# Performance work log

Measured on AMD Instinct MI355X. Metric: run time of the kernel, lower is better.

Reference implementation:

```python
import jax, jax.numpy as jnp
import numpy as np

CTX = 2048
D_IN = 2048
D_OUT = 2048
N_HEADS = 16
HEAD_DIM = D_OUT // N_HEADS
ROPE_BASE = 10000.0


def rope_tables(head_dim, ctx):
    inv_freq = 1.0 / (ROPE_BASE ** (jnp.arange(0, head_dim, 2, dtype=jnp.float32) / head_dim))
    angles = jnp.arange(ctx, dtype=jnp.float32)[:, None] * inv_freq[None, :]  # [ctx, hd/2]
    angles = jnp.concatenate([angles, angles], axis=1)  # [ctx, hd]
    return jnp.sin(angles), jnp.cos(angles)


def apply_rope(x, sin, cos):
    # x: [b, h, s, d]; rotate-by-half (Raschka / Llama style)
    s = x.shape[2]
    d = x.shape[3]
    x1, x2 = x[..., : d // 2], x[..., d // 2 :]
    rotated = jnp.concatenate([-x2, x1], axis=-1)
    return x * cos[:s][None, None] + rotated * sin[:s][None, None]


def setup_inputs() -> dict:
    key = jax.random.key(0)
    kx, kq, kk, kv, ko = jax.random.split(key, 5)
    scale = 0.02
    return {
        "x": jax.random.normal(kx, (2, CTX, D_IN), dtype=jnp.float32),
        "W_query": jax.random.normal(kq, (D_IN, D_OUT), dtype=jnp.float32) * scale,
        "W_key": jax.random.normal(kk, (D_IN, D_OUT), dtype=jnp.float32) * scale,
        "W_value": jax.random.normal(kv, (D_IN, D_OUT), dtype=jnp.float32) * scale,
        "W_out": jax.random.normal(ko, (D_OUT, D_OUT), dtype=jnp.float32) * scale,
    }


def reference(x, W_query, W_key, W_value, W_out):
    bs, cl, _ = x.shape
    sin, cos = rope_tables(HEAD_DIM, CTX)

    def split_heads(t):  # [b, s, d_out] -> [b, h, s, hd]
        return t.reshape(bs, cl, N_HEADS, HEAD_DIM).transpose(0, 2, 1, 3)

    q = split_heads(x @ W_query)
    k = split_heads(x @ W_key)
    v = split_heads(x @ W_value)

    q = apply_rope(q, sin, cos)
    k = apply_rope(k, sin, cos)

    # NOTE: original module does NOT scale by 1/sqrt(head_dim)
    scores = jnp.einsum("bhqd,bhkd->bhqk", q, k)
    causal = jnp.triu(jnp.ones((cl, cl), dtype=bool), k=1)
    scores = jnp.where(causal[None, None], -jnp.inf, scores)
    weights = jax.nn.softmax(scores, axis=-1)
    ctx = jnp.einsum("bhqk,bhkd->bhqd", weights, v)
    ctx = ctx.transpose(0, 2, 1, 3).reshape(bs, cl, N_HEADS * HEAD_DIM)
    return ctx @ W_out
```

## Files before the change

### kernel.cpp

```cpp
#include <hip/hip_runtime.h>
#include <cstdint>
#include <cstddef>

typedef _Float16 f16;
typedef _Float16 f16x8 __attribute__((ext_vector_type(8)));
typedef _Float16 f16x4 __attribute__((ext_vector_type(4)));
typedef float    f32x4 __attribute__((ext_vector_type(4)));

#define S_CTX 2048
#define NH 16
#define DH 128

#define BAR() asm volatile("s_barrier" ::: "memory")
#define VMW(n) asm volatile("s_waitcnt vmcnt(" #n ")" ::: "memory")
#define MF(a, b, c) __builtin_amdgcn_mfma_f32_16x16x32_f16((a), (b), (c), 0, 0, 0)

__device__ __forceinline__ void gload16(const void* g, void* l) {
  __builtin_amdgcn_global_load_lds(
      (const __attribute__((address_space(1))) void*)g,
      (__attribute__((address_space(3))) void*)l, 16, 0, 0);
}

__global__ void prep(const float* __restrict__ x,
                     const float* __restrict__ w0, const float* __restrict__ w1,
                     const float* __restrict__ w2, const float* __restrict__ w3,
                     f16* __restrict__ xb,
                     f16* __restrict__ o0, f16* __restrict__ o1,
                     f16* __restrict__ o2, f16* __restrict__ o3,
                     float* __restrict__ sint, float* __restrict__ cost) {
  const int bid = blockIdx.x, tid = threadIdx.x;
  if (bid < 512) {
    int idx = bid * 256 + tid;
    int j = idx & 63, s = idx >> 6;
    float invf = __expf(-(float)(2 * j) * (1.0f / 128.0f) * 9.210340371976184f);
    float a = (float)s * invf;
    sint[idx] = sinf(a);
    cost[idx] = cosf(a);
  } else if (bid < 8704) {
    int i = ((bid - 512) * 256 + tid) * 4;
    float4 v = *(const float4*)(x + i);
    f16x4 o; o[0] = (f16)v.x; o[1] = (f16)v.y; o[2] = (f16)v.z; o[3] = (f16)v.w;
    *(f16x4*)(xb + i) = o;
  } else {
    int b2 = bid - 8704;
    int z = b2 >> 12, rem = b2 & 4095;
    int by = rem >> 6, bx = rem & 63;
    int tx = tid & 31, ty = tid >> 5;
    const float* in; f16* out;
    switch (z) {
      case 0: in = w0; out = o0; break;
      case 1: in = w1; out = o1; break;
      case 2: in = w2; out = o2; break;
      default: in = w3; out = o3; break;
    }
    __shared__ float tl[32][33];
    int xc = bx * 32 + tx, yc = by * 32 + ty;
#pragma unroll
    for (int r = 0; r < 32; r += 8)
      tl[ty + r][tx] = in[(size_t)(yc + r) * 2048 + xc];
    __syncthreads();
    int xo = by * 32 + tx, yo = bx * 32 + ty;
#pragma unroll
    for (int r = 0; r < 32; r += 8)
      out[(size_t)(yo + r) * 2048 + xo] = (f16)tl[tx][ty + r];
  }
}

__global__ __launch_bounds__(512, 1)
void gemm_qk(const f16* __restrict__ A, const f16* __restrict__ wqT,
             const f16* __restrict__ wkT,
             f16* __restrict__ qb, f16* __restrict__ kb,
             const float* __restrict__ sint, const float* __restrict__ cost) {
  extern __shared__ __align__(16) char lds[];
  const int tid = threadIdx.x, lane = tid & 63;
  const int wvi = tid >> 6, wm = wvi >> 2, wn = wvi & 3;
  const int gcol = blockIdx.x * 256;
  const int proj = gcol >> 11;
  const int col0 = gcol & 2047;
  const int row0 = blockIdx.y * 256;
  const f16* Bt = proj ? wkT : wqT;

  const int ca0 = tid, ca1 = tid + 512;
  const int ra0 = ca0 >> 2, ra1 = ca1 >> 2;
  const int sa0 = (ca0 & 3) ^ ((ra0 >> 1) & 3);
  const int sa1 = (ca1 & 3) ^ ((ra1 >> 1) & 3);
  const f16* gA0 = A + (size_t)(row0 + ra0) * 2048 + sa0 * 8;
  const f16* gA1 = A + (size_t)(row0 + ra1) * 2048 + sa1 * 8;
  const f16* gB0 = Bt + (size_t)(col0 + ra0) * 2048 + sa0 * 8;
  const f16* gB1 = Bt + (size_t)(col0 + ra1) * 2048 + sa1 * 8;

  const int kslot = lane >> 4;
  int aoff[8], boff[4];
#pragma unroll
  for (int i = 0; i < 8; i++) {
    int row = wm * 128 + i * 16 + (lane & 15);
    aoff[i] = row * 64 + ((kslot ^ ((row >> 1) & 3)) << 4);
  }
#pragma unroll
  for (int j = 0; j < 4; j++) {
    int rb = (wn >> 1) * 128 + (wn & 1) * 32 + (j & 1) * 16 + (j >> 1) * 64 + (lane & 15);
    boff[j] = rb * 64 + ((kslot ^ ((rb >> 1) & 3)) << 4);
  }

  f32x4 acc[8][4] = {};

#define QKPH(SLOT, HS, SSLOT, DOSTAGE, WN) do {                                \
    const char* As_ = lds + (SLOT) * 32768;                                    \
    const char* Bs_ = As_ + 16384;                                             \
    f16x8 af[8], bf[4];                                                        \
    _Pragma("unroll") for (int i_ = 0; i_ < 8; i_++)                           \
      af[i_] = *(const f16x8*)(As_ + aoff[i_]);                                \
    _Pragma("unroll") for (int j_ = 0; j_ < 4; j_++)                           \
      bf[j_] = *(const f16x8*)(Bs_ + boff[j_]);                                \
    if (DOSTAGE) {                                                             \
      char* dA = lds + (SSLOT) * 32768;                                        \
      gload16(gA0 + (HS) * 32, dA + ca0 * 16);                                 \
      gload16(gA1 + (HS) * 32, dA + ca1 * 16);                                 \
      gload16(gB0 + (HS) * 32, dA + 16384 + ca0 * 16);                         \
      gload16(gB1 + (HS) * 32, dA + 16384 + ca1 * 16);                         \
    }                                                                          \
    asm volatile("s_waitcnt vmcnt(" #WN ")" ::: "memory");                     \
    BAR();                                                                     \
    __builtin_amdgcn_s_setprio(1);                                             \
    _Pragma("unroll") for (int i_ = 0; i_ < 8; i_++)                           \
      _Pragma("unroll") for (int j_ = 0; j_ < 4; j_++)                         \
        acc[i_][j_] = MF(af[i_], bf[j_], acc[i_][j_]);                         \
    __builtin_amdgcn_s_setprio(0);                                             \
    BAR();                                                                     \
  } while (0)

#pragma unroll
  for (int h = 0; h < 2; h++) {
    char* dA = lds + h * 32768;
    gload16(gA0 + h * 32, dA + ca0 * 16);
    gload16(gA1 + h * 32, dA + ca1 * 16);
    gload16(gB0 + h * 32, dA + 16384 + ca0 * 16);
    gload16(gB1 + h * 32, dA + 16384 + ca1 * 16);
  }
  VMW(4); BAR();

  for (int t = 0; t < 20; ++t) {
    const int hb = 3 * t;
    QKPH(0, hb + 2, 2, 1, 4);
    QKPH(1, hb + 3, 0, 1, 4);
    QKPH(2, hb + 4, 1, 1, 4);
  }
  QKPH(0, 62, 2, 1, 4);
  QKPH(1, 63, 0, 1, 4);
  QKPH(2, 0, 0, 0, 0);
  QKPH(0, 0, 0, 0, 63);
#undef QKPH

  const int b = row0 >> 11, sb = row0 & 2047;
  f16* dst = proj ? kb : qb;
  const int h = (col0 >> 7) + (wn >> 1);
#pragma unroll
  for (int i = 0; i < 8; i++)
#pragma unroll
    for (int jj = 0; jj < 2; jj++)
#pragma unroll
      for (int r = 0; r < 4; r++) {
        int s = sb + wm * 128 + i * 16 + (lane >> 4) * 4 + r;
        int d = (wn & 1) * 32 + jj * 16 + (lane & 15);
        float cv = cost[s * 64 + d], sv = sint[s * 64 + d];
        float x1 = acc[i][jj][r], x2 = acc[i][jj + 2][r];
        size_t base = ((size_t)(b * NH + h) * S_CTX + s) << 7;
        dst[base + d]      = (f16)(x1 * cv - x2 * sv);
        dst[base + d + 64] = (f16)(x2 * cv + x1 * sv);
      }
}

template<int MODE>
__global__ __launch_bounds__(512, 1)
void gemm8(const f16* __restrict__ A, const f16* __restrict__ Bt,
           f16* __restrict__ vtb, float* __restrict__ of) {
  extern __shared__ __align__(16) char lds[];
#define RING_A(e) (lds + (e) * 16384)
#define RING_B(e) (lds + 65536 + (e) * 8192)
  const int tid = threadIdx.x, lane = tid & 63;
  const int wvi = tid >> 6, wm = wvi >> 1, wn = wvi & 1;
  const int col0 = blockIdx.x * 128;
  const int row0 = blockIdx.y * 256;

  const int ca0 = tid, ca1 = tid + 512, cb0 = tid;
  const int rAs0 = ca0 >> 2, rAs1 = ca1 >> 2, rBs0 = cb0 >> 2;
  const int sA0 = (ca0 & 3) ^ ((rAs0 >> 1) & 3);
  const int sA1 = (ca1 & 3) ^ ((rAs1 >> 1) & 3);
  const int sB0 = (cb0 & 3) ^ ((rBs0 >> 1) & 3);
  const f16* gA0 = A + (size_t)(row0 + rAs0) * 2048 + sA0 * 8;
  const f16* gA1 = A + (size_t)(row0 + rAs1) * 2048 + sA1 * 8;
  const f16* gB0 = Bt + (size_t)(col0 + rBs0) * 2048 + sB0 * 8;

  const int kslot = lane >> 4;
  int aoff[4], boff[4];
#pragma unroll
  for (int i = 0; i < 4; i++) {
    int row = wm * 64 + i * 16 + (lane & 15);
    aoff[i] = row * 64 + ((kslot ^ ((row >> 1) & 3)) << 4);
  }
#pragma unroll
  for (int j = 0; j < 4; j++) {
    int rb = wn * 32 + (j & 1) * 16 + (j >> 1) * 64 + (lane & 15);
    boff[j] = rb * 64 + ((kslot ^ ((rb >> 1) & 3)) << 4);
  }

  f32x4 acc[4][4] = {};

#define PH8(SLOT, HS, DOSTAGE, WN) do {                                        \
    const char* As_ = RING_A(SLOT);                                            \
    const char* Bs_ = RING_B(SLOT);                                            \
    f16x8 af[4], bf[4];                                                        \
    _Pragma("unroll") for (int i_ = 0; i_ < 4; i_++)                           \
      af[i_] = *(const f16x8*)(As_ + aoff[i_]);                                \
    _Pragma("unroll") for (int j_ = 0; j_ < 4; j_++)                           \
      bf[j_] = *(const f16x8*)(Bs_ + boff[j_]);                                \
    if (DOSTAGE) {                                                             \
      gload16(gA0 + (HS) * 32, RING_A((HS) & 3) + ca0 * 16);                   \
      gload16(gA1 + (HS) * 32, RING_A((HS) & 3) + ca1 * 16);                   \
      gload16(gB0 + (HS) * 32, RING_B((HS) & 3) + cb0 * 16);                   \
    }                                                                          \
    asm volatile("s_waitcnt vmcnt(" #WN ")" ::: "memory");                     \
    BAR();                                                                     \
    __builtin_amdgcn_s_setprio(1);                                             \
    _Pragma("unroll") for (int i_ = 0; i_ < 4; i_++)                           \
      _Pragma("unroll") for (int j_ = 0; j_ < 4; j_++)                         \
        acc[i_][j_] = MF(af[i_], bf[j_], acc[i_][j_]);                         \
    __builtin_amdgcn_s_setprio(0);                                             \
    BAR();                                                                     \
  } while (0)

#pragma unroll
  for (int h = 0; h < 3; h++) {
    gload16(gA0 + h * 32, RING_A(h) + ca0 * 16);
    gload16(gA1 + h * 32, RING_A(h) + ca1 * 16);
    gload16(gB0 + h * 32, RING_B(h) + cb0 * 16);
  }
  VMW(6); BAR();

  for (int t = 0; t < 15; ++t) {
    const int p = t * 4;
    PH8(0, p + 3, 1, 6);
    PH8(1, p + 4, 1, 6);
    PH8(2, p + 5, 1, 6);
    PH8(3, p + 6, 1, 6);
  }
  PH8(0, 63, 1, 6);
  PH8(1, 0, 0, 3);
  PH8(2, 0, 0, 0);
  PH8(3, 0, 0, 63);
#undef PH8

  const int b = row0 >> 11, sbase = row0 & 2047;

  if (MODE == 2) {
#pragma unroll
    for (int i = 0; i < 4; i++)
#pragma unroll
      for (int j = 0; j < 4; j++)
#pragma unroll
        for (int r = 0; r < 4; r++) {
          int row = row0 + wm * 64 + i * 16 + (lane >> 4) * 4 + r;
          int col = col0 + wn * 32 + (j & 1) * 16 + (j >> 1) * 64 + (lane & 15);
          of[(size_t)row * 2048 + col] = acc[i][j][r];
        }
  } else {
    const int h = col0 >> 7;
    f16x4* ldsv = (f16x4*)lds;
#pragma unroll
    for (int i = 0; i < 4; i++)
#pragma unroll
      for (int j = 0; j < 4; j++) {
        f16x4 v;
#pragma unroll
        for (int r = 0; r < 4; r++) v[r] = (f16)acc[i][j][r];
        int su = wm * 16 + i * 4 + (lane >> 4);
        int d  = wn * 32 + (j & 1) * 16 + (j >> 1) * 64 + (lane & 15);
        ldsv[d * 64 + (su ^ ((d << 1) & 63))] = v;
      }
    __syncthreads();
#pragma unroll
    for (int it = 0; it < 8; ++it) {
      int o = it * 512 + tid;
      int d = o >> 5, c = o & 31;
      int xc = (d << 1) & 63;
      f16x4 lo = ldsv[d * 64 + ((2 * c) ^ xc)];
      f16x4 hi = ldsv[d * 64 + ((2 * c + 1) ^ xc)];
      f16x8 vv;
      vv[0] = lo[0]; vv[1] = lo[1]; vv[2] = lo[2]; vv[3] = lo[3];
      vv[4] = hi[0]; vv[5] = hi[1]; vv[6] = hi[2]; vv[7] = hi[3];
      *(f16x8*)&vtb[((size_t)(b * NH + h) * DH + d) * S_CTX + sbase + c * 8] = vv;
    }
  }
#undef RING_A
#undef RING_B
}

__global__ __launch_bounds__(512)
void attn_k(const f16* __restrict__ q, const f16* __restrict__ kk,
            const f16* __restrict__ vt, f16* __restrict__ ctx) {
  __shared__ __align__(16) f16 Ks[2][64 * 128];
  __shared__ __align__(16) f16 Vs[2][128 * 64];
  __shared__ __align__(16) f16 Pl[8][16 * 64];
  const int tid = threadIdx.x, lane = tid & 63, wv = tid >> 6;
  const int bid = blockIdx.x;
  const int xcd = bid & 7, rr = bid >> 3;
  const int bh = xcd + 8 * (rr & 3);
  const int qp = rr >> 2;
  const int b = bh >> 4, h = bh & 15;
  const size_t plane = (size_t)bh * (S_CTX * DH);
  const f16* Qp = q + plane;
  const f16* Kp = kk + plane;
  const f16* Vp = vt + plane;
  const float LOG2E = 1.4426950408889634f;

  const int ck0 = tid, ck1 = tid + 512;
  const int cv0 = tid, cv1 = tid + 512;

  for (int half = 0; half < 2; half++) {
    const int Q = half ? (15 - qp) : qp;
    const int q0 = Q * 128;
    const int NT = 2 * Q + 2;

    f16x8 qf[4];
    {
      const f16* qq = Qp + (size_t)(q0 + wv * 16 + (lane & 15)) * DH + ((lane >> 4) * 8);
#pragma unroll
      for (int ks = 0; ks < 4; ks++) {
        qf[ks] = *(const f16x8*)(qq + ks * 32);
#pragma unroll
        for (int e = 0; e < 8; e++) qf[ks][e] = (f16)((float)qf[ks][e] * LOG2E);
      }
    }
    float m_[4], l_[4];
    f32x4 o[8] = {};
#pragma unroll
    for (int r = 0; r < 4; r++) { m_[r] = -3e38f; l_[r] = 0.f; }

    {
      int rk0 = ck0 >> 4, rk1 = ck1 >> 4;
      gload16(Kp + (size_t)rk0 * DH + (((ck0 & 15) ^ (rk0 & 7)) * 8), &Ks[0][ck0 * 8]);
      gload16(Kp + (size_t)rk1 * DH + (((ck1 & 15) ^ (rk1 & 7)) * 8), &Ks[0][ck1 * 8]);
      int rv0 = cv0 >> 3, rv1 = cv1 >> 3;
      gload16(Vp + (size_t)rv0 * S_CTX + (((cv0 & 7) ^ (rv0 & 7)) * 8), &Vs[0][cv0 * 8]);
      gload16(Vp + (size_t)rv1 * S_CTX + (((cv1 & 7) ^ (rv1 & 7)) * 8), &Vs[0][cv1 * 8]);
    }
    VMW(0); BAR();

    int cur = 0;
    for (int t = 0; t < NT; t++) {
      if (t + 1 < NT) {
        const f16* Kt = Kp + (size_t)(t + 1) * 64 * DH;
        const f16* Vt = Vp + (size_t)(t + 1) * 64;
        int nb = cur ^ 1;
        int rk0 = ck0 >> 4, rk1 = ck1 >> 4;
        gload16(Kt + (size_t)rk0 * DH + (((ck0 & 15) ^ (rk0 & 7)) * 8), &Ks[nb][ck0 * 8]);
        gload16(Kt + (size_t)rk1 * DH + (((ck1 & 15) ^ (rk1 & 7)) * 8), &Ks[nb][ck1 * 8]);
        int rv0 = cv0 >> 3, rv1 = cv1 >> 3;
        gload16(Vt + (size_t)rv0 * S_CTX + (((cv0 & 7) ^ (rv0 & 7)) * 8), &Vs[nb][cv0 * 8]);
        gload16(Vt + (size_t)rv1 * S_CTX + (((cv1 & 7) ^ (rv1 & 7)) * 8), &Vs[nb][cv1 * 8]);
      }

      const f16* Ksc = Ks[cur];
      const f16* Vsc = Vs[cur];

      f32x4 st[4] = {};
      __builtin_amdgcn_s_setprio(1);
#pragma unroll
      for (int n = 0; n < 4; n++) {
        int rK = n * 16 + (lane & 15);
#pragma unroll
        for (int ks = 0; ks < 4; ks++) {
          int slot = ks * 4 + (lane >> 4);
          f16x8 kf = *(const f16x8*)&Ksc[rK * 128 + ((slot ^ (rK & 7)) << 3)];
          st[n] = MF(qf[ks], kf, st[n]);
        }
      }
      __builtin_amdgcn_s_setprio(0);
      if (t >= 2 * Q) {
#pragma unroll
        for (int n = 0; n < 4; n++)
#pragma unroll
          for (int r = 0; r < 4; r++) {
            int kvc = t * 64 + n * 16 + (lane & 15);
            int qr = q0 + wv * 16 + (lane >> 4) * 4 + r;
            if (kvc > qr) st[n][r] = -3e38f;
          }
      }
      float mx[4];
#pragma unroll
      for (int r = 0; r < 4; r++)
        mx[r] = fmaxf(fmaxf(st[0][r], st[1][r]), fmaxf(st[2][r], st[3][r]));
#pragma unroll
      for (int msk = 1; msk < 16; msk <<= 1)
#pragma unroll
        for (int r = 0; r < 4; r++) mx[r] = fmaxf(mx[r], __shfl_xor(mx[r], msk));
      bool need = false;
#pragma unroll
      for (int r = 0; r < 4; r++) need = need || (mx[r] > m_[r] + 8.0f);
      if (__any(need)) {
#pragma unroll
        for (int r = 0; r < 4; r++) {
          float nm = fmaxf(m_[r], mx[r]);
          float al = __builtin_amdgcn_exp2f(m_[r] - nm);
          m_[r] = nm;
          l_[r] *= al;
#pragma unroll
          for (int j = 0; j < 8; j++) o[j][r] *= al;
        }
      }
      float ps[4] = {0.f, 0.f, 0.f, 0.f};
      float pvv[4][4];
#pragma unroll
      for (int n = 0; n < 4; n++)
#pragma unroll
        for (int r = 0; r < 4; r++) {
          float p = __builtin_amdgcn_exp2f(st[n][r] - m_[r]);
          pvv[n][r] = p; ps[r] += p;
        }
#pragma unroll
      for (int msk = 1; msk < 16; msk <<= 1)
#pragma unroll
        for (int r = 0; r < 4; r++) ps[r] += __shfl_xor(ps[r], msk);
#pragma unroll
      for (int r = 0; r < 4; r++) l_[r] += ps[r];

      f16* Pw = Pl[wv];
#pragma unroll
      for (int n = 0; n < 4; n++)
#pragma unroll
        for (int r = 0; r < 4; r++) {
          int rowp = (lane >> 4) * 4 + r;
          int colp = n * 16 + (lane & 15);
          Pw[rowp * 64 + (((colp >> 3) ^ (rowp & 7)) << 3) + (colp & 7)] = (f16)pvv[n][r];
        }
      __builtin_amdgcn_s_setprio(1);
#pragma unroll
      for (int ks = 0; ks < 2; ks++) {
        int rowp = lane & 15;
        int slotp = ks * 4 + (lane >> 4);
        f16x8 pa = *(const f16x8*)&Pw[rowp * 64 + ((slotp ^ (rowp & 7)) << 3)];
#pragma unroll
        for (int j = 0; j < 8; j++) {
          int rv = j * 16 + (lane & 15);
          int slotv = ks * 4 + (lane >> 4);
          f16x8 vf = *(const f16x8*)&Vsc[rv * 64 + ((slotv ^ (rv & 7)) << 3)];
          o[j] = MF(pa, vf, o[j]);
        }
      }
      __builtin_amdgcn_s_setprio(0);

      VMW(0); BAR();
      cur ^= 1;
    }

#pragma unroll
    for (int j = 0; j < 8; j++)
#pragma unroll
      for (int r = 0; r < 4; r++) {
        int qr = q0 + wv * 16 + (lane >> 4) * 4 + r;
        int dd = h * 128 + j * 16 + (lane & 15);
        ctx[((size_t)(b * S_CTX + qr) * 2048) + dd] = (f16)(o[j][r] / l_[r]);
      }
  }
}

extern "C" void kernel_launch(void* const* d_in, const int* in_sizes, int n_in,
                              void* d_out, int out_size, void* d_ws, size_t ws_size,
                              hipStream_t stream) {
  (void)in_sizes; (void)n_in; (void)out_size; (void)ws_size;
  const float* x  = (const float*)d_in[0];
  const float* Wq = (const float*)d_in[1];
  const float* Wk = (const float*)d_in[2];
  const float* Wv = (const float*)d_in[3];
  const float* Wo = (const float*)d_in[4];
  float* out = (float*)d_out;
  char* ws = (char*)d_ws;

  f16*   xb   = (f16*)(ws);
  f16*   ctxb = (f16*)(ws);
  f16*   wqT  = (f16*)(ws + 16777216);
  f16*   wkT  = (f16*)(ws + 25165824);
  f16*   wvT  = (f16*)(ws + 33554432);
  f16*   woT  = (f16*)(ws + 41943040);
  f16*   qb   = (f16*)(ws + 50331648);
  f16*   kb   = (f16*)(ws + 67108864);
  f16*   vtb  = (f16*)(ws + 83886080);
  float* sint = (float*)(ws + 100663296);
  float* cost = (float*)(ws + 101187584);

  prep<<<dim3(25088), dim3(256), 0, stream>>>(x, Wq, Wk, Wv, Wo, xb,
                                              wqT, wkT, wvT, woT, sint, cost);
  gemm_qk<<<dim3(16, 16), dim3(512), 98304, stream>>>(xb, wqT, wkT, qb, kb, sint, cost);
  gemm8<1><<<dim3(16, 16), dim3(512), 98304, stream>>>(xb, wvT, vtb, nullptr);
  attn_k<<<dim3(256), dim3(512), 0, stream>>>(qb, kb, vtb, ctxb);
  gemm8<2><<<dim3(16, 16), dim3(512), 98304, stream>>>(ctxb, woT, nullptr, out);
}
```

Before: 273.4 us.

## Rewrite attention with 32x32 MFMA, register-resident P, and per-block q-tile grid

The attention kernel moves from 16x16x32 to 32x32x16 MFMA and computes S transposed (K times Q), so the P fragments can be packed to f16 and rearranged with v_permlane32_swap in registers instead of going through a per-wave LDS scratch buffer. Blocks shrink to 4 waves of 32 query rows each, and the grid doubles to 512 blocks with one q-tile per block, replacing the paired causal-balancing loop, with launch bounds asking for 2 blocks per CU. This cuts LDS traffic and shuffle reductions, but drops the explicit load balancing of causal tiles and relies on the hardware scheduler and occupancy instead.

```diff
diff --git a/kernel.cpp b/kernel.cpp
--- a/kernel.cpp
+++ b/kernel.cpp
@@ -6,6 +6,8 @@
 typedef _Float16 f16x8 __attribute__((ext_vector_type(8)));
 typedef _Float16 f16x4 __attribute__((ext_vector_type(4)));
 typedef float    f32x4 __attribute__((ext_vector_type(4)));
+typedef float    f32x16 __attribute__((ext_vector_type(16)));
+typedef int      i32x4 __attribute__((ext_vector_type(4)));
 
 #define S_CTX 2048
 #define NH 16
@@ -14,11 +16,20 @@
 #define BAR() asm volatile("s_barrier" ::: "memory")
 #define VMW(n) asm volatile("s_waitcnt vmcnt(" #n ")" ::: "memory")
 #define MF(a, b, c) __builtin_amdgcn_mfma_f32_16x16x32_f16((a), (b), (c), 0, 0, 0)
+#define MF32(a, b, c) __builtin_amdgcn_mfma_f32_32x32x16_f16((a), (b), (c), 0, 0, 0)
 
 __device__ __forceinline__ void gload16(const void* g, void* l) {
   __builtin_amdgcn_global_load_lds(
       (const __attribute__((address_space(1))) void*)g,
       (__attribute__((address_space(3))) void*)l, 16, 0, 0);
+}
+
+__device__ __forceinline__ int pk2(float a, float b) {
+  auto hv = __builtin_amdgcn_cvt_pkrtz(a, b);
+  return __builtin_bit_cast(int, hv);
+}
+__device__ __forceinline__ void pl_swap(int& a, int& b) {
+  asm volatile("v_permlane32_swap_b32 %0, %1" : "+v"(a), "+v"(b));
 }
 
 __global__ void prep(const float* __restrict__ x,
@@ -295,172 +306,157 @@
 #undef RING_B
 }
 
-__global__ __launch_bounds__(512)
+__global__ __launch_bounds__(256, 2)
 void attn_k(const f16* __restrict__ q, const f16* __restrict__ kk,
             const f16* __restrict__ vt, f16* __restrict__ ctx) {
   __shared__ __align__(16) f16 Ks[2][64 * 128];
   __shared__ __align__(16) f16 Vs[2][128 * 64];
-  __shared__ __align__(16) f16 Pl[8][16 * 64];
   const int tid = threadIdx.x, lane = tid & 63, wv = tid >> 6;
+  const int lh = lane >> 5, q31 = lane & 31;
   const int bid = blockIdx.x;
   const int xcd = bid & 7, rr = bid >> 3;
   const int bh = xcd + 8 * (rr & 3);
-  const int qp = rr >> 2;
+  const int Q = 15 - (rr >> 2);
   const int b = bh >> 4, h = bh & 15;
   const size_t plane = (size_t)bh * (S_CTX * DH);
   const f16* Qp = q + plane;
   const f16* Kp = kk + plane;
   const f16* Vp = vt + plane;
   const float LOG2E = 1.4426950408889634f;
-
-  const int ck0 = tid, ck1 = tid + 512;
-  const int cv0 = tid, cv1 = tid + 512;
-
-  for (int half = 0; half < 2; half++) {
-    const int Q = half ? (15 - qp) : qp;
-    const int q0 = Q * 128;
-    const int NT = 2 * Q + 2;
-
-    f16x8 qf[4];
+  const int q0 = Q * 128;
+  const int NT = 2 * Q + 2;
+
+#define STAGE(T, BUF) do {                                                      \
+    const f16* Kt = Kp + (size_t)(T) * 64 * DH;                                 \
+    const f16* Vt = Vp + (size_t)(T) * 64;                                      \
+    _Pragma("unroll") for (int j_ = 0; j_ < 4; j_++) {                          \
+      int c = tid + j_ * 256; int rk = c >> 4;                                  \
+      gload16(Kt + (size_t)rk * DH + (((c & 15) ^ (rk & 7)) * 8), &Ks[BUF][c * 8]); \
+    }                                                                           \
+    _Pragma("unroll") for (int j_ = 0; j_ < 4; j_++) {                          \
+      int c = tid + j_ * 256; int rv = c >> 3;                                  \
+      gload16(Vt + (size_t)rv * S_CTX + (((c & 7) ^ (rv & 7)) * 8), &Vs[BUF][c * 8]); \
+    }                                                                           \
+  } while (0)
+
+  f16x8 qf[8];
+  {
+    const f16* qq = Qp + (size_t)(q0 + wv * 32 + q31) * DH + lh * 8;
+#pragma unroll
+    for (int s = 0; s < 8; s++) {
+      qf[s] = *(const f16x8*)(qq + s * 16);
+#pragma unroll
+      for (int e = 0; e < 8; e++) qf[s][e] = (f16)((float)qf[s][e] * LOG2E);
+    }
+  }
+  float m_ = -3e38f, l_ = 0.f;
+  f32x16 o[4] = {};
+
+  STAGE(0, 0);
+  VMW(0); BAR();
+
+  int cur = 0;
+  for (int t = 0; t < NT; t++) {
+    if (t + 1 < NT) {
+      if (cur) STAGE(t + 1, 0); else STAGE(t + 1, 1);
+    }
+    const f16* Ksc = Ks[cur];
+    const f16* Vsc = Vs[cur];
+
+    f32x16 st0 = {}, st1 = {};
+    __builtin_amdgcn_s_setprio(1);
+#pragma unroll
+    for (int s = 0; s < 8; s++) {
+      const int r0 = q31, r1 = 32 + q31;
+      f16x8 kf0 = *(const f16x8*)&Ksc[r0 * 128 + (((2 * s + lh) ^ (r0 & 7)) << 3)];
+      f16x8 kf1 = *(const f16x8*)&Ksc[r1 * 128 + (((2 * s + lh) ^ (r1 & 7)) << 3)];
+      st0 = MF32(kf0, qf[s], st0);
+      st1 = MF32(kf1, qf[s], st1);
+    }
+    __builtin_amdgcn_s_setprio(0);
+
+    if (t >= 2 * Q) {
+      const int qg = q0 + wv * 32 + q31;
+#pragma unroll
+      for (int r = 0; r < 16; r++) {
+        int kvb = t * 64 + (r & 3) + 8 * (r >> 2) + 4 * lh;
+        if (kvb > qg) st0[r] = -3e38f;
+        if (kvb + 32 > qg) st1[r] = -3e38f;
+      }
+    }
+    float mx = st0[0];
+#pragma unroll
+    for (int r = 1; r < 16; r++) mx = fmaxf(mx, st0[r]);
+#pragma unroll
+    for (int r = 0; r < 16; r++) mx = fmaxf(mx, st1[r]);
+    mx = fmaxf(mx, __shfl_xor(mx, 32));
+    if (__any(mx > m_ + 8.0f)) {
+      float nm = fmaxf(m_, mx);
+      float al = __builtin_amdgcn_exp2f(m_ - nm);
+      m_ = nm; l_ *= al;
+#pragma unroll
+      for (int r = 0; r < 16; r++) {
+        float alr = __shfl(al, (r & 3) + 8 * (r >> 2) + 4 * lh);
+#pragma unroll
+        for (int j = 0; j < 4; j++) o[j][r] *= alr;
+      }
+    }
+    float s_ = 0.f;
+#pragma unroll
+    for (int r = 0; r < 16; r++) { st0[r] = __builtin_amdgcn_exp2f(st0[r] - m_); s_ += st0[r]; }
+#pragma unroll
+    for (int r = 0; r < 16; r++) { st1[r] = __builtin_amdgcn_exp2f(st1[r] - m_); s_ += st1[r]; }
+    s_ += __shfl_xor(s_, 32);
+    l_ += s_;
+
+    f16x8 pa[4];
     {
-      const f16* qq = Qp + (size_t)(q0 + wv * 16 + (lane & 15)) * DH + ((lane >> 4) * 8);
-#pragma unroll
-      for (int ks = 0; ks < 4; ks++) {
-        qf[ks] = *(const f16x8*)(qq + ks * 32);
-#pragma unroll
-        for (int e = 0; e < 8; e++) qf[ks][e] = (f16)((float)qf[ks][e] * LOG2E);
+      int w0 = pk2(st0[0], st0[1]),   w1 = pk2(st0[2], st0[3]);
+      int w2 = pk2(st0[4], st0[5]),   w3 = pk2(st0[6], st0[7]);
+      int w4 = pk2(st0[8], st0[9]),   w5 = pk2(st0[10], st0[11]);
+      int w6 = pk2(st0[12], st0[13]), w7 = pk2(st0[14], st0[15]);
+      pl_swap(w0, w2); pl_swap(w1, w3); pl_swap(w4, w6); pl_swap(w5, w7);
+      i32x4 a = {w0, w1, w2, w3}; pa[0] = __builtin_bit_cast(f16x8, a);
+      i32x4 bb = {w4, w5, w6, w7}; pa[1] = __builtin_bit_cast(f16x8, bb);
+    }
+    {
+      int w0 = pk2(st1[0], st1[1]),   w1 = pk2(st1[2], st1[3]);
+      int w2 = pk2(st1[4], st1[5]),   w3 = pk2(st1[6], st1[7]);
+      int w4 = pk2(st1[8], st1[9]),   w5 = pk2(st1[10], st1[11]);
+      int w6 = pk2(st1[12], st1[13]), w7 = pk2(st1[14], st1[15]);
+      pl_swap(w0, w2); pl_swap(w1, w3); pl_swap(w4, w6); pl_swap(w5, w7);
+      i32x4 a = {w0, w1, w2, w3}; pa[2] = __builtin_bit_cast(f16x8, a);
+      i32x4 bb = {w4, w5, w6, w7}; pa[3] = __builtin_bit_cast(f16x8, bb);
+    }
+
+    __builtin_amdgcn_s_setprio(1);
+#pragma unroll
+    for (int j = 0; j < 4; j++) {
+      const int rv = 32 * j + q31;
+#pragma unroll
+      for (int s2 = 0; s2 < 4; s2++) {
+        f16x8 vf = *(const f16x8*)&Vsc[rv * 64 + (((2 * s2 + lh) ^ (rv & 7)) << 3)];
+        o[j] = MF32(pa[s2], vf, o[j]);
       }
     }
-    float m_[4], l_[4];
-    f32x4 o[8] = {};
-#pragma unroll
-    for (int r = 0; r < 4; r++) { m_[r] = -3e38f; l_[r] = 0.f; }
-
-    {
-      int rk0 = ck0 >> 4, rk1 = ck1 >> 4;
-      gload16(Kp + (size_t)rk0 * DH + (((ck0 & 15) ^ (rk0 & 7)) * 8), &Ks[0][ck0 * 8]);
-      gload16(Kp + (size_t)rk1 * DH + (((ck1 & 15) ^ (rk1 & 7)) * 8), &Ks[0][ck1 * 8]);
-      int rv0 = cv0 >> 3, rv1 = cv1 >> 3;
-      gload16(Vp + (size_t)rv0 * S_CTX + (((cv0 & 7) ^ (rv0 & 7)) * 8), &Vs[0][cv0 * 8]);
-      gload16(Vp + (size_t)rv1 * S_CTX + (((cv1 & 7) ^ (rv1 & 7)) * 8), &Vs[0][cv1 * 8]);
-    }
+    __builtin_amdgcn_s_setprio(0);
+
     VMW(0); BAR();
-
-    int cur = 0;
-    for (int t = 0; t < NT; t++) {
-      if (t + 1 < NT) {
-        const f16* Kt = Kp + (size_t)(t + 1) * 64 * DH;
-        const f16* Vt = Vp + (size_t)(t + 1) * 64;
-        int nb = cur ^ 1;
-        int rk0 = ck0 >> 4, rk1 = ck1 >> 4;
-        gload16(Kt + (size_t)rk0 * DH + (((ck0 & 15) ^ (rk0 & 7)) * 8), &Ks[nb][ck0 * 8]);
-        gload16(Kt + (size_t)rk1 * DH + (((ck1 & 15) ^ (rk1 & 7)) * 8), &Ks[nb][ck1 * 8]);
-        int rv0 = cv0 >> 3, rv1 = cv1 >> 3;
-        gload16(Vt + (size_t)rv0 * S_CTX + (((cv0 & 7) ^ (rv0 & 7)) * 8), &Vs[nb][cv0 * 8]);
-        gload16(Vt + (size_t)rv1 * S_CTX + (((cv1 & 7) ^ (rv1 & 7)) * 8), &Vs[nb][cv1 * 8]);
-      }
-
-      const f16* Ksc = Ks[cur];
-      const f16* Vsc = Vs[cur];
-
-      f32x4 st[4] = {};
-      __builtin_amdgcn_s_setprio(1);
-#pragma unroll
-      for (int n = 0; n < 4; n++) {
-        int rK = n * 16 + (lane & 15);
-#pragma unroll
-        for (int ks = 0; ks < 4; ks++) {
-          int slot = ks * 4 + (lane >> 4);
-          f16x8 kf = *(const f16x8*)&Ksc[rK * 128 + ((slot ^ (rK & 7)) << 3)];
-          st[n] = MF(qf[ks], kf, st[n]);
-        }
-      }
-      __builtin_amdgcn_s_setprio(0);
-      if (t >= 2 * Q) {
-#pragma unroll
-        for (int n = 0; n < 4; n++)
-#pragma unroll
-          for (int r = 0; r < 4; r++) {
-            int kvc = t * 64 + n * 16 + (lane & 15);
-            int qr = q0 + wv * 16 + (lane >> 4) * 4 + r;
-            if (kvc > qr) st[n][r] = -3e38f;
-          }
-      }
-      float mx[4];
-#pragma unroll
-      for (int r = 0; r < 4; r++)
-        mx[r] = fmaxf(fmaxf(st[0][r], st[1][r]), fmaxf(st[2][r], st[3][r]));
-#pragma unroll
-      for (int msk = 1; msk < 16; msk <<= 1)
-#pragma unroll
-        for (int r = 0; r < 4; r++) mx[r] = fmaxf(mx[r], __shfl_xor(mx[r], msk));
-      bool need = false;
-#pragma unroll
-      for (int r = 0; r < 4; r++) need = need || (mx[r] > m_[r] + 8.0f);
-      if (__any(need)) {
-#pragma unroll
-        for (int r = 0; r < 4; r++) {
-          float nm = fmaxf(m_[r], mx[r]);
-          float al = __builtin_amdgcn_exp2f(m_[r] - nm);
-          m_[r] = nm;
-          l_[r] *= al;
-#pragma unroll
-          for (int j = 0; j < 8; j++) o[j][r] *= al;
-        }
-      }
-      float ps[4] = {0.f, 0.f, 0.f, 0.f};
-      float pvv[4][4];
-#pragma unroll
-      for (int n = 0; n < 4; n++)
-#pragma unroll
-        for (int r = 0; r < 4; r++) {
-          float p = __builtin_amdgcn_exp2f(st[n][r] - m_[r]);
-          pvv[n][r] = p; ps[r] += p;
-        }
-#pragma unroll
-      for (int msk = 1; msk < 16; msk <<= 1)
-#pragma unroll
-        for (int r = 0; r < 4; r++) ps[r] += __shfl_xor(ps[r], msk);
-#pragma unroll
-      for (int r = 0; r < 4; r++) l_[r] += ps[r];
-
-      f16* Pw = Pl[wv];
-#pragma unroll
-      for (int n = 0; n < 4; n++)
-#pragma unroll
-        for (int r = 0; r < 4; r++) {
-          int rowp = (lane >> 4) * 4 + r;
-          int colp = n * 16 + (lane & 15);
-          Pw[rowp * 64 + (((colp >> 3) ^ (rowp & 7)) << 3) + (colp & 7)] = (f16)pvv[n][r];
-        }
-      __builtin_amdgcn_s_setprio(1);
-#pragma unroll
-      for (int ks = 0; ks < 2; ks++) {
-        int rowp = lane & 15;
-        int slotp = ks * 4 + (lane >> 4);
-        f16x8 pa = *(const f16x8*)&Pw[rowp * 64 + ((slotp ^ (rowp & 7)) << 3)];
-#pragma unroll
-        for (int j = 0; j < 8; j++) {
-          int rv = j * 16 + (lane & 15);
-          int slotv = ks * 4 + (lane >> 4);
-          f16x8 vf = *(const f16x8*)&Vsc[rv * 64 + ((slotv ^ (rv & 7)) << 3)];
-          o[j] = MF(pa, vf, o[j]);
-        }
-      }
-      __builtin_amdgcn_s_setprio(0);
-
-      VMW(0); BAR();
-      cur ^= 1;
-    }
-
-#pragma unroll
-    for (int j = 0; j < 8; j++)
-#pragma unroll
-      for (int r = 0; r < 4; r++) {
-        int qr = q0 + wv * 16 + (lane >> 4) * 4 + r;
-        int dd = h * 128 + j * 16 + (lane & 15);
-        ctx[((size_t)(b * S_CTX + qr) * 2048) + dd] = (f16)(o[j][r] / l_[r]);
-      }
+    cur ^= 1;
+  }
+#undef STAGE
+
+  float inv = 1.0f / l_;
+#pragma unroll
+  for (int r = 0; r < 16; r++) {
+    int crow = (r & 3) + 8 * (r >> 2) + 4 * lh;
+    float invr = __shfl(inv, crow);
+    int qg = q0 + wv * 32 + crow;
+#pragma unroll
+    for (int j = 0; j < 4; j++) {
+      int dd = h * 128 + 32 * j + q31;
+      ctx[((size_t)(b * S_CTX + qg) * 2048) + dd] = (f16)(o[j][r] * invr);
+    }
   }
 }
 
@@ -492,6 +488,6 @@
                                               wqT, wkT, wvT, woT, sint, cost);
   gemm_qk<<<dim3(16, 16), dim3(512), 98304, stream>>>(xb, wqT, wkT, qb, kb, sint, cost);
   gemm8<1><<<dim3(16, 16), dim3(512), 98304, stream>>>(xb, wvT, vtb, nullptr);
-  attn_k<<<dim3(256), dim3(512), 0, stream>>>(qb, kb, vtb, ctxb);
+  attn_k<<<dim3(512), dim3(256), 0, stream>>>(qb, kb, vtb, ctxb);
   gemm8<2><<<dim3(16, 16), dim3(512), 98304, stream>>>(ctxb, woT, nullptr, out);
 }
```

Result: faster. 248.7 us (-9.0%).
